# Kernel optimization log

Hardware: AMD Instinct MI355X
Metric: run time of the kernel (lower is better)

Reference implementation:

```python
import jax, jax.numpy as jnp
import numpy as np

BOTTLENECK_DIM = 128
TOP_K = 8
SCALE = 1.0 / np.sqrt(BOTTLENECK_DIM)
EPS = 1e-10


def setup_inputs() -> dict:
    key = jax.random.key(0)
    k1, k2, k3, k4 = jax.random.split(key, 4)
    query = jax.random.normal(k1, (4, 4096, 128), dtype=jnp.float32)
    keys = jax.random.normal(k2, (4096, 128), dtype=jnp.float32)
    values = jax.random.normal(k3, (4096, 1024), dtype=jnp.float32)
    reliability = jax.random.uniform(k4, (4096,), dtype=jnp.float32)
    return {"query": query, "keys": keys, "values": values, "reliability": reliability}


def reference(query, keys, values, reliability):
    # Routing: [b, s, num_slots] scores with log-reliability bias, take top-k slots.
    router_scores = jnp.einsum("bsd,nd->bsn", query, keys) + jnp.log(reliability + EPS)
    _, top_indices = jax.lax.top_k(router_scores, TOP_K)  # [b, s, k]

    # Gather per-token slot keys/values: [b, s, k, d] and [b, s, k, h]
    selected_keys = keys[top_indices]
    selected_values = values[top_indices]

    # Small-k attention over gathered slots.
    attn_scores = jnp.einsum("bsd,bskd->bsk", query, selected_keys) * SCALE
    attn_weights = jax.nn.softmax(attn_scores, axis=-1)  # [b, s, k]
    output = jnp.einsum("bsk,bskh->bsh", attn_weights, selected_values)
    return output, attn_weights
```

## Files before the change

kernel.cpp:

```cpp
#include <hip/hip_runtime.h>
#include <hip/hip_fp16.h>
#include <math.h>

#define NSLOTS 4096
#define DIM    128
#define HDIM   1024
#define NTOK   16384
#define SCALE  0.08838834764831845f
#define REPS   1e-10f

typedef __attribute__((ext_vector_type(8))) short bf16x8;
typedef __attribute__((ext_vector_type(4))) float f32x4;

__device__ __forceinline__ float pack_score(float biased, unsigned inv_idx) {
    return __uint_as_float((__float_as_uint(biased) & 0xFFFFF000u) | inv_idx);
}
#define PACK_NEG_INF __uint_as_float(0xFF7FF000u)

__device__ __forceinline__ void ins_packed(float (&r)[8], float x) {
    #pragma unroll
    for (int i = 0; i < 7; ++i) r[i] = __builtin_amdgcn_fmed3f(r[i], x, r[i + 1]);
    r[7] = fmaxf(r[7], x);
}

__device__ __forceinline__ void merge_out16(float (&r)[8], int kseg, float* outS) {
    float hv = r[7];
    #pragma unroll
    for (int rnd = 0; rnd < 16; ++rnd) {
        float bv = hv;
        bv = fmaxf(bv, __shfl_xor(bv, 16, 64));
        bv = fmaxf(bv, __shfl_xor(bv, 32, 64));
        if ((rnd >> 2) == kseg) outS[rnd] = bv;
        if (hv == bv) {
            #pragma unroll
            for (int m2 = 7; m2 > 0; --m2) r[m2] = r[m2 - 1];
            r[0] = PACK_NEG_INF;
            hv = r[7];
        }
    }
}

__device__ __forceinline__ ushort f2bf(float f) {
    unsigned u = __float_as_uint(f);
    return (ushort)((u + 0x7fffu + ((u >> 16) & 1u)) >> 16);
}
#define QB_N  524288
#define KBP_N 65536
#define LR_N  4096
#define VH_N  524288
__global__ void prep_kernel(const float* __restrict__ q, const float* __restrict__ k,
                            const float* __restrict__ rel, const float* __restrict__ v,
                            ushort* __restrict__ qb, ushort* __restrict__ kbp,
                            float* __restrict__ lr, ushort* __restrict__ vh) {
    int gid = blockIdx.x * 256 + threadIdx.x;
    if (gid < QB_N) {
        float4 vv = ((const float4*)q)[gid];
        ushort4 o; o.x = f2bf(vv.x); o.y = f2bf(vv.y); o.z = f2bf(vv.z); o.w = f2bf(vv.w);
        ((ushort4*)qb)[gid] = o;
    } else if (gid < QB_N + KBP_N) {
        int C = gid - QB_N;
        int l = C & 63, kc = (C >> 6) & 3, t16 = C >> 8;
        int slot = t16 * 16 + (l & 15);
        int doff = kc * 32 + (l >> 4) * 8;
        const float4* src = (const float4*)(k + (size_t)slot * DIM + doff);
        float4 v0 = src[0], v1 = src[1];
        union { ushort u[8]; uint4 v; } o;
        o.u[0] = f2bf(v0.x); o.u[1] = f2bf(v0.y); o.u[2] = f2bf(v0.z); o.u[3] = f2bf(v0.w);
        o.u[4] = f2bf(v1.x); o.u[5] = f2bf(v1.y); o.u[6] = f2bf(v1.z); o.u[7] = f2bf(v1.w);
        ((uint4*)kbp)[C] = o.v;
    } else if (gid < QB_N + KBP_N + LR_N) {
        int g = gid - QB_N - KBP_N;
        lr[g] = logf(rel[g] + REPS);
    } else if (gid < QB_N + KBP_N + LR_N + VH_N) {
        int g = gid - QB_N - KBP_N - LR_N;
        int slot = g >> 7;
        int d0   = (g & 127) * 8;
        const float4* src = (const float4*)v + (size_t)g * 2;
        float4 a = src[0], b = src[1];
        union { _Float16 h[8]; uint4 u; } o;
        o.h[0] = (_Float16)a.x; o.h[1] = (_Float16)a.y;
        o.h[2] = (_Float16)a.z; o.h[3] = (_Float16)a.w;
        o.h[4] = (_Float16)b.x; o.h[5] = (_Float16)b.y;
        o.h[6] = (_Float16)b.z; o.h[7] = (_Float16)b.w;
        size_t didx = (d0 < 512)
            ? ((size_t)slot * 64 + (d0 >> 3))
            : ((size_t)4096 * 64 + (size_t)slot * 64 + ((d0 - 512) >> 3));
        ((uint4*)vh)[didx] = o.u;
    }
}

__launch_bounds__(512, 4)
__global__ void route_kernel(const ushort* __restrict__ qb,
                             const ushort* __restrict__ kbp,
                             const float*  __restrict__ lr,
                             int* __restrict__ cand) {
    __shared__ float qS[32][8][17];
    const int tid  = threadIdx.x;
    const int lane = tid & 63;
    const int w    = tid >> 6;
    const int m    = lane & 15;
    const int kseg = lane >> 4;
    const int tokbase = blockIdx.x * 32;

    bf16x8 bF0[4], bF1[4];
    const ushort* q0 = qb + (size_t)(tokbase + m) * DIM + kseg * 8;
    const ushort* q1 = qb + (size_t)(tokbase + 16 + m) * DIM + kseg * 8;
    #pragma unroll
    for (int kc = 0; kc < 4; ++kc) {
        bF0[kc] = *(const bf16x8*)(q0 + kc * 32);
        bF1[kc] = *(const bf16x8*)(q1 + kc * 32);
    }

    float R0[8], R1[8];
    #pragma unroll
    for (int i = 0; i < 8; ++i) { R0[i] = PACK_NEG_INF; R1[i] = PACK_NEG_INF; }

    const uint4* kb4 = (const uint4*)kbp;
    const int tbase = w * 32;

    uint4 A[4], N[4];
    #pragma unroll
    for (int kc = 0; kc < 4; ++kc)
        A[kc] = kb4[(size_t)tbase * 256 + kc * 64 + lane];

    for (int t = 0; t < 32; ++t) {
        if (t < 31) {
            #pragma unroll
            for (int kc = 0; kc < 4; ++kc)
                N[kc] = kb4[(size_t)(tbase + t + 1) * 256 + kc * 64 + lane];
        }
        f32x4 acc0 = {0.f, 0.f, 0.f, 0.f};
        f32x4 acc1 = {0.f, 0.f, 0.f, 0.f};
        #pragma unroll
        for (int kc = 0; kc < 4; ++kc) {
            bf16x8 aF = *(const bf16x8*)&A[kc];
            acc0 = __builtin_amdgcn_mfma_f32_16x16x32_bf16(aF, bF0[kc], acc0, 0, 0, 0);
            acc1 = __builtin_amdgcn_mfma_f32_16x16x32_bf16(aF, bF1[kc], acc1, 0, 0, 0);
        }
        const int base = w * 512 + t * 16;
        float4 lrv = ((const float4*)lr)[(base >> 2) + kseg];
        unsigned invb = 4095u - (unsigned)(base + kseg * 4);
        ins_packed(R0, pack_score(acc0[0] + lrv.x, invb));
        ins_packed(R0, pack_score(acc0[1] + lrv.y, invb - 1));
        ins_packed(R0, pack_score(acc0[2] + lrv.z, invb - 2));
        ins_packed(R0, pack_score(acc0[3] + lrv.w, invb - 3));
        ins_packed(R1, pack_score(acc1[0] + lrv.x, invb));
        ins_packed(R1, pack_score(acc1[1] + lrv.y, invb - 1));
        ins_packed(R1, pack_score(acc1[2] + lrv.z, invb - 2));
        ins_packed(R1, pack_score(acc1[3] + lrv.w, invb - 3));
        #pragma unroll
        for (int kc = 0; kc < 4; ++kc) A[kc] = N[kc];
    }

    merge_out16(R0, kseg, &qS[m][w][0]);
    merge_out16(R1, kseg, &qS[m + 16][w][0]);
    __syncthreads();

    if (tid < 32) {
        const int token = tokbase + tid;
        int p[8] = {0, 0, 0, 0, 0, 0, 0, 0};
        #pragma unroll
        for (int c = 0; c < 16; ++c) {
            float bv = -INFINITY; int bq = 0;
            #pragma unroll
            for (int j = 0; j < 8; ++j) {
                float v = (p[j] < 16) ? qS[tid][j][p[j]] : -INFINITY;
                if (v > bv) { bv = v; bq = j; }
            }
            cand[(size_t)token * 16 + c] = 4095 - (int)(__float_as_uint(bv) & 0xFFFu);
            ++p[bq];
        }
    }
}

__launch_bounds__(256)
__global__ void score_kernel(const float* __restrict__ query,
                             const float* __restrict__ keys,
                             const float* __restrict__ lr,
                             const int*   __restrict__ cand,
                             int*   __restrict__ iselg,
                             float* __restrict__ wout) {
    const int tid  = threadIdx.x;
    const int w    = tid >> 6;
    const int lane = tid & 63;
    const int token = blockIdx.x * 4 + w;
    const int c  = lane >> 2;
    const int qp = lane & 3;

    int ci = cand[(size_t)token * 16 + c];
    const float4* q4 = (const float4*)(query + (size_t)token * DIM) + qp * 8;
    const float4* k4 = (const float4*)(keys  + (size_t)ci    * DIM) + qp * 8;
    float sum = 0.f;
    #pragma unroll
    for (int i = 0; i < 8; ++i) {
        float4 a = q4[i], b = k4[i];
        sum = fmaf(a.x, b.x, sum); sum = fmaf(a.y, b.y, sum);
        sum = fmaf(a.z, b.z, sum); sum = fmaf(a.w, b.w, sum);
    }
    sum += __shfl_xor(sum, 1, 4);
    sum += __shfl_xor(sum, 2, 4);
    float raw = sum;
    float s   = sum + lr[ci];

    #pragma unroll
    for (int k = 2; k <= 16; k <<= 1) {
        #pragma unroll
        for (int j = k >> 1; j >= 1; j >>= 1) {
            int off = j << 2;
            float s2 = __shfl_xor(s,   off, 64);
            float r2 = __shfl_xor(raw, off, 64);
            int   i2 = __shfl_xor(ci,  off, 64);
            bool mineFirst = (s > s2) || (s == s2 && ci < i2);
            bool lower = (c & j) == 0;
            bool asc   = (c & k) == 0;
            bool keep  = (lower == asc) ? mineFirst : !mineFirst;
            if (!keep) { s = s2; raw = r2; ci = i2; }
        }
    }
    float rsel[8]; int isel[8];
    #pragma unroll
    for (int r = 0; r < 8; ++r) {
        rsel[r] = __shfl(raw, r * 4, 64);
        isel[r] = __shfl(ci,  r * 4, 64);
    }

    float mx = -INFINITY;
    #pragma unroll
    for (int k = 0; k < 8; ++k) { rsel[k] *= SCALE; mx = fmaxf(mx, rsel[k]); }
    float e[8]; float ssum = 0.f;
    #pragma unroll
    for (int k = 0; k < 8; ++k) { e[k] = expf(rsel[k] - mx); ssum += e[k]; }
    float inv = 1.0f / ssum;

    if (lane == 0) {
        float4* wo = (float4*)(wout + (size_t)token * 8);
        wo[0] = make_float4(e[0] * inv, e[1] * inv, e[2] * inv, e[3] * inv);
        wo[1] = make_float4(e[4] * inv, e[5] * inv, e[6] * inv, e[7] * inv);
        int4* io = (int4*)(iselg + (size_t)token * 8);
        io[0] = make_int4(isel[0], isel[1], isel[2], isel[3]);
        io[1] = make_int4(isel[4], isel[5], isel[6], isel[7]);
    }
}

__device__ __forceinline__ float2 h2f2(unsigned u) {
    return __half22float2(*reinterpret_cast<const __half2*>(&u));
}
__launch_bounds__(256)
__global__ void gather_kernel(const float* __restrict__ wout,
                              const int*   __restrict__ iselg,
                              const ushort* __restrict__ vh,
                              float* __restrict__ out) {
    const int tid  = threadIdx.x;
    const int wv   = tid >> 6;
    const int lane = tid & 63;
    const int b    = blockIdx.x;
    const int x    = b & 7;
    const int dhalf = x >> 2;
    const int tg   = (b >> 3) * 4 + (x & 3);
    const int token = tg * 4 + wv;

    const float4* wo = (const float4*)(wout + (size_t)token * 8);
    const int4*   io = (const int4*)(iselg + (size_t)token * 8);
    float4 w0 = wo[0], w1 = wo[1];
    int4   i0 = io[0], i1 = io[1];

    const uint4* vbase = (const uint4*)vh + (size_t)dhalf * 4096 * 64;
    uint4 va[8];
    va[0] = vbase[(size_t)i0.x * 64 + lane];
    va[1] = vbase[(size_t)i0.y * 64 + lane];
    va[2] = vbase[(size_t)i0.z * 64 + lane];
    va[3] = vbase[(size_t)i0.w * 64 + lane];
    va[4] = vbase[(size_t)i1.x * 64 + lane];
    va[5] = vbase[(size_t)i1.y * 64 + lane];
    va[6] = vbase[(size_t)i1.z * 64 + lane];
    va[7] = vbase[(size_t)i1.w * 64 + lane];
    float wk[8] = {w0.x, w0.y, w0.z, w0.w, w1.x, w1.y, w1.z, w1.w};

    float o[8];
    #pragma unroll
    for (int i = 0; i < 8; ++i) o[i] = 0.f;
    #pragma unroll
    for (int k = 0; k < 8; ++k) {
        float wkk = wk[k];
        float2 f;
        f = h2f2(va[k].x); o[0] = fmaf(wkk, f.x, o[0]); o[1] = fmaf(wkk, f.y, o[1]);
        f = h2f2(va[k].y); o[2] = fmaf(wkk, f.x, o[2]); o[3] = fmaf(wkk, f.y, o[3]);
        f = h2f2(va[k].z); o[4] = fmaf(wkk, f.x, o[4]); o[5] = fmaf(wkk, f.y, o[5]);
        f = h2f2(va[k].w); o[6] = fmaf(wkk, f.x, o[6]); o[7] = fmaf(wkk, f.y, o[7]);
    }
    f32x4* orow = (f32x4*)(out + (size_t)token * HDIM + dhalf * 512 + lane * 8);
    f32x4 s0 = {o[0], o[1], o[2], o[3]};
    f32x4 s1 = {o[4], o[5], o[6], o[7]};
    __builtin_nontemporal_store(s0, orow);
    __builtin_nontemporal_store(s1, orow + 1);
}

extern "C" void kernel_launch(void* const* d_in, const int* in_sizes, int n_in,
                              void* d_out, int out_size, void* d_ws, size_t ws_size,
                              hipStream_t stream) {
    const float* query  = (const float*)d_in[0];
    const float* keys   = (const float*)d_in[1];
    const float* values = (const float*)d_in[2];
    const float* rel    = (const float*)d_in[3];

    float* out  = (float*)d_out;
    float* wout = out + (size_t)NTOK * HDIM;

    char* ws = (char*)d_ws;
    float*  lr    = (float*)ws;   ws += 4096 * 4;
    ushort* qb    = (ushort*)ws;  ws += (size_t)NTOK * DIM * 2;
    ushort* kbp   = (ushort*)ws;  ws += (size_t)NSLOTS * DIM * 2;
    int*    cand  = (int*)ws;     ws += (size_t)NTOK * 16 * 4;
    int*    iselg = (int*)ws;     ws += (size_t)NTOK * 8 * 4;
    ushort* vh    = (ushort*)ws;

    int prep_grid = (QB_N + KBP_N + LR_N + VH_N) / 256;
    hipLaunchKernelGGL(prep_kernel, dim3(prep_grid), dim3(256), 0, stream,
                       query, keys, rel, values, qb, kbp, lr, vh);
    hipLaunchKernelGGL(route_kernel, dim3(NTOK / 32), dim3(512), 0, stream,
                       qb, kbp, lr, cand);
    hipLaunchKernelGGL(score_kernel, dim3(NTOK / 4), dim3(256), 0, stream,
                       query, keys, lr, cand, iselg, wout);
    hipLaunchKernelGGL(gather_kernel, dim3(NTOK / 2), dim3(256), 0, stream,
                       wout, iselg, vh, out);
}
```

Measured before the change: 189.5 us.

## Split routing slot range across two blocks and merge candidate pools in score kernel

```diff
diff --git a/kernel.cpp b/kernel.cpp
--- a/kernel.cpp
+++ b/kernel.cpp
@@ -89,18 +89,20 @@
     }
 }
 
-__launch_bounds__(512, 4)
+__launch_bounds__(512, 8)
 __global__ void route_kernel(const ushort* __restrict__ qb,
                              const ushort* __restrict__ kbp,
                              const float*  __restrict__ lr,
-                             int* __restrict__ cand) {
+                             float* __restrict__ cpool) {
     __shared__ float qS[32][8][17];
     const int tid  = threadIdx.x;
     const int lane = tid & 63;
     const int w    = tid >> 6;
     const int m    = lane & 15;
     const int kseg = lane >> 4;
-    const int tokbase = blockIdx.x * 32;
+    const int tg   = blockIdx.x >> 1;
+    const int half = blockIdx.x & 1;
+    const int tokbase = tg * 32;
 
     bf16x8 bF0[4], bF1[4];
     const ushort* q0 = qb + (size_t)(tokbase + m) * DIM + kseg * 8;
@@ -116,15 +118,15 @@
     for (int i = 0; i < 8; ++i) { R0[i] = PACK_NEG_INF; R1[i] = PACK_NEG_INF; }
 
     const uint4* kb4 = (const uint4*)kbp;
-    const int tbase = w * 32;
+    const int tbase = half * 128 + w * 16;
 
     uint4 A[4], N[4];
     #pragma unroll
     for (int kc = 0; kc < 4; ++kc)
         A[kc] = kb4[(size_t)tbase * 256 + kc * 64 + lane];
 
-    for (int t = 0; t < 32; ++t) {
-        if (t < 31) {
+    for (int t = 0; t < 16; ++t) {
+        if (t < 15) {
             #pragma unroll
             for (int kc = 0; kc < 4; ++kc)
                 N[kc] = kb4[(size_t)(tbase + t + 1) * 256 + kc * 64 + lane];
@@ -137,7 +139,7 @@
             acc0 = __builtin_amdgcn_mfma_f32_16x16x32_bf16(aF, bF0[kc], acc0, 0, 0, 0);
             acc1 = __builtin_amdgcn_mfma_f32_16x16x32_bf16(aF, bF1[kc], acc1, 0, 0, 0);
         }
-        const int base = w * 512 + t * 16;
+        const int base = half * 2048 + w * 256 + t * 16;
         float4 lrv = ((const float4*)lr)[(base >> 2) + kseg];
         unsigned invb = 4095u - (unsigned)(base + kseg * 4);
         ins_packed(R0, pack_score(acc0[0] + lrv.x, invb));
@@ -167,7 +169,7 @@
                 float v = (p[j] < 16) ? qS[tid][j][p[j]] : -INFINITY;
                 if (v > bv) { bv = v; bq = j; }
             }
-            cand[(size_t)token * 16 + c] = 4095 - (int)(__float_as_uint(bv) & 0xFFFu);
+            cpool[(size_t)token * 32 + half * 16 + c] = bv;
             ++p[bq];
         }
     }
@@ -177,17 +179,33 @@
 __global__ void score_kernel(const float* __restrict__ query,
                              const float* __restrict__ keys,
                              const float* __restrict__ lr,
-                             const int*   __restrict__ cand,
+                             const float* __restrict__ cpool,
                              int*   __restrict__ iselg,
                              float* __restrict__ wout) {
     const int tid  = threadIdx.x;
     const int w    = tid >> 6;
     const int lane = tid & 63;
     const int token = blockIdx.x * 4 + w;
+    const int c5 = lane & 31;
+
+    float pv = cpool[(size_t)token * 32 + c5];
+    #pragma unroll
+    for (int k = 2; k <= 32; k <<= 1) {
+        #pragma unroll
+        for (int j = k >> 1; j >= 1; j >>= 1) {
+            float p2 = __shfl_xor(pv, j, 64);
+            bool mineFirst = pv > p2;
+            bool lower = (c5 & j) == 0;
+            bool asc   = (c5 & k) == 0;
+            bool keep  = (lower == asc) ? mineFirst : !mineFirst;
+            if (!keep) pv = p2;
+        }
+    }
+    float pc = __shfl(pv, lane >> 2, 64);
+    int ci = 4095 - (int)(__float_as_uint(pc) & 0xFFFu);
+
     const int c  = lane >> 2;
     const int qp = lane & 3;
-
-    int ci = cand[(size_t)token * 16 + c];
     const float4* q4 = (const float4*)(query + (size_t)token * DIM) + qp * 8;
     const float4* k4 = (const float4*)(keys  + (size_t)ci    * DIM) + qp * 8;
     float sum = 0.f;
@@ -310,17 +328,17 @@
     float*  lr    = (float*)ws;   ws += 4096 * 4;
     ushort* qb    = (ushort*)ws;  ws += (size_t)NTOK * DIM * 2;
     ushort* kbp   = (ushort*)ws;  ws += (size_t)NSLOTS * DIM * 2;
-    int*    cand  = (int*)ws;     ws += (size_t)NTOK * 16 * 4;
+    float*  cpool = (float*)ws;   ws += (size_t)NTOK * 32 * 4;
     int*    iselg = (int*)ws;     ws += (size_t)NTOK * 8 * 4;
     ushort* vh    = (ushort*)ws;
 
     int prep_grid = (QB_N + KBP_N + LR_N + VH_N) / 256;
     hipLaunchKernelGGL(prep_kernel, dim3(prep_grid), dim3(256), 0, stream,
                        query, keys, rel, values, qb, kbp, lr, vh);
-    hipLaunchKernelGGL(route_kernel, dim3(NTOK / 32), dim3(512), 0, stream,
-                       qb, kbp, lr, cand);
+    hipLaunchKernelGGL(route_kernel, dim3(NTOK / 32 * 2), dim3(512), 0, stream,
+                       qb, kbp, lr, cpool);
     hipLaunchKernelGGL(score_kernel, dim3(NTOK / 4), dim3(256), 0, stream,
-                       query, keys, lr, cand, iselg, wout);
+                       query, keys, lr, cpool, iselg, wout);
     hipLaunchKernelGGL(gather_kernel, dim3(NTOK / 2), dim3(256), 0, stream,
                        wout, iselg, vh, out);
 }
```

Measured after the change: 247.1 us. 30.4% more time.
